# Kernel tuning notes

Hardware: AMD Instinct MI355X
Metric: run time of the kernel (lower is better)

Reference implementation:

```python
import jax, jax.numpy as jnp
import numpy as np

B, N, C = 4, 2048, 1024


def setup_inputs() -> dict:
    key = jax.random.key(0)
    ks = jax.random.split(key, 5)
    s = 1.0 / np.sqrt(C)
    return {
        "event_f": jax.random.normal(ks[0], (B, N, C), dtype=jnp.float32),
        "img_f": jax.random.normal(ks[1], (B, N, C), dtype=jnp.float32),
        "Wq": jax.random.normal(ks[2], (C, C), dtype=jnp.float32) * s,
        "bq": jnp.zeros((C,), dtype=jnp.float32),
        "Wk": jax.random.normal(ks[3], (C, C), dtype=jnp.float32) * s,
        "bk": jnp.zeros((C,), dtype=jnp.float32),
        "Wv": jax.random.normal(ks[4], (C, C), dtype=jnp.float32) * s,
        "bv": jnp.zeros((C,), dtype=jnp.float32),
    }


def reference(event_f, img_f, Wq, bq, Wk, bk, Wv, bv):
    # pointwise projections (conv_query/key/val as 1x1 / Linear C->C)
    q = jnp.einsum("bnc,cd->bnd", event_f, Wq) + bq  # [B,N,C]
    k = jnp.einsum("bnc,cd->bnd", img_f, Wk) + bk
    v = jnp.einsum("bnc,cd->bnd", img_f, Wv) + bv
    scale = 1.0 / jnp.sqrt(jnp.asarray(q.shape[-1], dtype=q.dtype))
    scores = jnp.einsum("bqc,bkc->bqk", q, k) * scale  # [B,N,N]
    p_attn = jax.nn.softmax(scores, axis=-1)
    return jnp.einsum("bqk,bkc->bqc", p_attn, v)  # [B,N,C]
```

## Files before the change

### kernel.cpp

```cpp
#include <hip/hip_runtime.h>
#include <hip/hip_bf16.h>
#include <stdint.h>

typedef __bf16 bf16;
typedef __attribute__((ext_vector_type(8))) __bf16 bf16x8;
typedef __attribute__((ext_vector_type(4))) float f32x4;

typedef __attribute__((address_space(3))) char* lds_ptr;
typedef const __attribute__((address_space(1))) char* glb_ptr;

#define BZ 4
#define NN 2048
#define CC 1024

__device__ __forceinline__ void gload_lds16(const bf16* g, bf16* l) {
    __builtin_amdgcn_global_load_lds((glb_ptr)g, (lds_ptr)l, 16, 0, 0);
}

__device__ __forceinline__ void bar() {
    asm volatile("" ::: "memory");
    __builtin_amdgcn_s_barrier();
    asm volatile("" ::: "memory");
}

__global__ void cvt2_f32_bf16(const float* __restrict__ a, const float* __restrict__ b,
                              bf16* __restrict__ oa, bf16* __restrict__ ob, int n8) {
    int i = blockIdx.x * blockDim.x + threadIdx.x;
    if (i >= 2 * n8) return;
    const float4* p;
    bf16* dst;
    int j;
    if (i < n8) { p = (const float4*)a; dst = oa; j = i; }
    else        { p = (const float4*)b; dst = ob; j = i - n8; }
    float4 x = p[2 * j], y = p[2 * j + 1];
    bf16x8 o;
    o[0] = (bf16)x.x; o[1] = (bf16)x.y; o[2] = (bf16)x.z; o[3] = (bf16)x.w;
    o[4] = (bf16)y.x; o[5] = (bf16)y.y; o[6] = (bf16)y.z; o[7] = (bf16)y.w;
    *(bf16x8*)(dst + 8 * (size_t)j) = o;
}

__global__ void transposeW3(const float* __restrict__ W0, const float* __restrict__ W1,
                            const float* __restrict__ W2, bf16* __restrict__ T0,
                            bf16* __restrict__ T1, bf16* __restrict__ T2) {
    __shared__ bf16 t[32][33];
    const int z = blockIdx.z;
    const float* W = z == 0 ? W0 : (z == 1 ? W1 : W2);
    bf16* Wt = z == 0 ? T0 : (z == 1 ? T1 : T2);
    int d0 = blockIdx.x * 32, c0 = blockIdx.y * 32;
    int tx = threadIdx.x, ty = threadIdx.y;
#pragma unroll
    for (int i = 0; i < 4; i++)
        t[ty + 8 * i][tx] = (bf16)W[(size_t)(c0 + ty + 8 * i) * CC + d0 + tx];
    __syncthreads();
#pragma unroll
    for (int i = 0; i < 4; i++)
        Wt[(size_t)(d0 + ty + 8 * i) * CC + c0 + tx] = t[tx][ty + 8 * i];
}

__global__ void prep(const float* __restrict__ a, const float* __restrict__ b,
                     float* __restrict__ bqk, float* __restrict__ rowsum) {
    int i = blockIdx.x * blockDim.x + threadIdx.x;
    rowsum[i] = 0.f;
    if (i < CC) bqk[i] = a[i];
    else if (i < 2 * CC) bqk[i] = b[i - CC];
}


#define STAGE_A(kt_, hh_)                                                        \
    do {                                                                         \
        int _kt = (kt_);                                                         \
        if (_kt < nkt) {                                                         \
            const bf16* _s = gAs + (size_t)((hh_)*128) * lda + (size_t)_kt * 64; \
            bf16* _d = &LA[_kt & 1][((hh_)*128 + wid * 16) * 64];                \
            gload_lds16(_s, _d);                                                 \
            gload_lds16(_s + (size_t)8 * lda, _d + 8 * 64);                      \
        }                                                                        \
    } while (0)

#define STAGE_B(kt_, hh_)                                                          \
    do {                                                                           \
        int _kt = (kt_);                                                           \
        if (_kt < nkt) {                                                           \
            const bf16* _s = gBs + (size_t)((hh_) * (BN / 2)) * ldb +              \
                             (size_t)_kt * 64;                                     \
            bf16* _d = &LB[_kt & 1][((hh_) * (BN / 2) + wid * (BN / 16)) * 64];    \
            gload_lds16(_s, _d);                                                   \
            if (NJ == 2) gload_lds16(_s + (size_t)8 * ldb, _d + 8 * 64);           \
        }                                                                          \
    } while (0)

#define LDA_FRAG(buf_, mh_)                                                      \
    do {                                                                         \
        _Pragma("unroll") for (int _i = 0; _i < 4; ++_i)                         \
            _Pragma("unroll") for (int _ks = 0; _ks < 2; ++_ks)                  \
                a[_i][_ks] = *(const bf16x8*)&LA[buf_][                          \
                    (wm + (mh_)*64 + _i * 16 + fr) * 64 +                        \
                    (((_ks * 4 + hi) ^ lo) * 8)];                                \
    } while (0)

#define LDB_FRAG(buf_, nh_, dst_)                                                \
    do {                                                                         \
        _Pragma("unroll") for (int _j = 0; _j < NJ; ++_j)                        \
            _Pragma("unroll") for (int _ks = 0; _ks < 2; ++_ks)                  \
                dst_[_j][_ks] = *(const bf16x8*)&LB[buf_][                       \
                    (wn + (nh_) * (NJ * 16) + _j * 16 + fr) * 64 +               \
                    (((_ks * 4 + hi) ^ lo) * 8)];                                \
    } while (0)

#define MMQ(mh_, nh_, b_)                                                        \
    do {                                                                         \
        __builtin_amdgcn_s_setprio(1);                                           \
        _Pragma("unroll") for (int _i = 0; _i < 4; ++_i)                         \
            _Pragma("unroll") for (int _j = 0; _j < NJ; ++_j)                    \
                _Pragma("unroll") for (int _ks = 0; _ks < 2; ++_ks)              \
                    acc[(mh_)*4 + _i][(nh_)*NJ + _j] =                           \
                        __builtin_amdgcn_mfma_f32_16x16x32_bf16(                 \
                            a[_i][_ks], b_[_j][_ks],                             \
                            acc[(mh_)*4 + _i][(nh_)*NJ + _j], 0, 0, 0);          \
        __builtin_amdgcn_s_setprio(0);                                           \
    } while (0)

#define VM_STEADY()                                                              \
    do {                                                                         \
        if (NJ == 2)                                                             \
            asm volatile("s_waitcnt vmcnt(6)" ::: "memory");                     \
        else                                                                     \
            asm volatile("s_waitcnt vmcnt(4)" ::: "memory");                     \
    } while (0)

template <int BN, int EPI, bool OUT_F32>
__global__ __launch_bounds__(512, 2) void gemm8(
    const bf16* __restrict__ A, int lda,
    const bf16* __restrict__ Bt, int ldb,
    void* __restrict__ Cout, int ldc,
    float* __restrict__ aux, long long sAux, float scale,
    long long sA, long long sB, long long sC, int nkt) {
    constexpr int NJ = BN / 128;
    __shared__ __align__(16) bf16 LA[2][256 * 64];
    __shared__ __align__(16) bf16 LB[2][BN * 64];

    const int nx = gridDim.x, ny = gridDim.y;
    const int nwg = nx * ny * gridDim.z;
    const int orig = blockIdx.x + nx * (blockIdx.y + ny * blockIdx.z);
    const int q = nwg >> 3, r = nwg & 7;
    const int xcd = orig & 7, land = orig >> 3;
    const int swz = (xcd < r ? xcd * (q + 1) : r * (q + 1) + (xcd - r) * q) + land;
    const int bx = swz % nx;
    const int tmp = swz / nx;
    const int by = tmp % ny, bz = tmp / ny;

    A += (size_t)bz * sA;
    Bt += (size_t)bz * sB;
    const int m0 = by * 256, n0 = bx * BN;
    const int t = threadIdx.x, wid = t >> 6, lane = t & 63;
    const int wm = (wid >> 2) * 128, wn = (wid & 3) * (BN / 4);
    const int fr = lane & 15, hi = lane >> 4, lo = lane & 7;
    f32x4 acc[8][2 * NJ] = {};

    const int srow = lane >> 3;
    const int schunk = lo ^ srow;
    const bf16* gAs = A + (size_t)(m0 + wid * 16 + srow) * lda + schunk * 8;
    const bf16* gBs = Bt + (size_t)(n0 + wid * (BN / 16) + srow) * ldb + schunk * 8;

    STAGE_A(0, 0); STAGE_A(0, 1); STAGE_B(0, 0); STAGE_B(0, 1);
    STAGE_B(1, 0); STAGE_A(1, 0); STAGE_B(1, 1);
    VM_STEADY();
    bar();

    bf16x8 a[4][2], b0[NJ][2], b1[NJ][2];
    for (int kt = 0; kt < nkt; ++kt) {
        const int buf = kt & 1;
        LDA_FRAG(buf, 0);
        LDB_FRAG(buf, 0, b0);
        STAGE_A(kt + 1, 1);
        MMQ(0, 0, b0);
        bar();
        LDB_FRAG(buf, 1, b1);
        MMQ(0, 1, b1);
        bar();
        LDA_FRAG(buf, 1);
        STAGE_B(kt + 2, 0);
        MMQ(1, 1, b1);
        bar();
        STAGE_A(kt + 2, 0);
        STAGE_B(kt + 2, 1);
        MMQ(1, 0, b0);
        if (kt + 2 < nkt)
            VM_STEADY();
        else
            asm volatile("s_waitcnt vmcnt(0)" ::: "memory");
        bar();
    }

    const int rq = hi * 4;
#pragma unroll
    for (int mh = 0; mh < 2; mh++)
#pragma unroll
        for (int i = 0; i < 4; i++) {
            const int row = m0 + wm + mh * 64 + i * 16 + rq;
            float rsum[4] = {0.f, 0.f, 0.f, 0.f};
            float inv[4];
            if (EPI == 4) {
#pragma unroll
                for (int rr = 0; rr < 4; rr++)
                    inv[rr] = 1.f / aux[bz * sAux + row + rr];
            }
#pragma unroll
            for (int nh = 0; nh < 2; nh++)
#pragma unroll
                for (int j = 0; j < NJ; j++) {
                    int col = n0 + wn + nh * (NJ * 16) + j * 16 + fr;
                    float bb = (EPI == 1) ? aux[bz * sAux + col] : 0.f;
                    f32x4 v = acc[mh * 4 + i][nh * NJ + j];
#pragma unroll
                    for (int rr = 0; rr < 4; rr++) {
                        float o = v[rr] * scale + bb;
                        if (EPI == 2) o += aux[row + rr];
                        if (EPI == 3) { o = __expf(o - 6.f); rsum[rr] += o; }
                        if (EPI == 4) o *= inv[rr];
                        if (OUT_F32)
                            ((float*)Cout)[(size_t)bz * sC + (size_t)(row + rr) * ldc + col] = o;
                        else
                            ((bf16*)Cout)[(size_t)bz * sC + (size_t)(row + rr) * ldc + col] = (bf16)o;
                    }
                }
            if (EPI == 3) {
#pragma unroll
                for (int rr = 0; rr < 4; rr++) {
                    float s = rsum[rr];
                    s += __shfl_xor(s, 1);
                    s += __shfl_xor(s, 2);
                    s += __shfl_xor(s, 4);
                    s += __shfl_xor(s, 8);
                    if (fr == 0) atomicAdd(&aux[bz * sAux + row + rr], s);
                }
            }
        }
}

extern "C" void kernel_launch(void* const* d_in, const int* in_sizes, int n_in,
                              void* d_out, int out_size, void* d_ws, size_t ws_size,
                              hipStream_t stream) {
    const float* event_f = (const float*)d_in[0];
    const float* img_f   = (const float*)d_in[1];
    const float* Wq = (const float*)d_in[2];
    const float* bq = (const float*)d_in[3];
    const float* Wk = (const float*)d_in[4];
    const float* bk = (const float*)d_in[5];
    const float* Wv = (const float*)d_in[6];
    const float* bv = (const float*)d_in[7];
    float* out = (float*)d_out;

    bf16* ws = (bf16*)d_ws;
    const size_t MC = (size_t)BZ * NN * CC;
    const size_t CCsq = (size_t)CC * CC;
    bf16* Ebf  = ws;
    bf16* Ibf  = ws + MC;
    bf16* S    = ws;
    size_t off = 2 * MC;
    bf16* Wqkt = ws + off; off += 2 * CCsq;
    bf16* Wvt  = ws + off; off += CCsq;
    bf16* Qb   = ws + off; off += MC;
    bf16* Kb   = ws + off; off += MC;
    bf16* VT   = ws + off; off += MC;
    float* bqk = (float*)(ws + off);
    float* rowsum = bqk + 2 * CC;

    {
        int n8 = (int)(MC / 8);
        cvt2_f32_bf16<<<dim3((2 * n8 + 255) / 256), dim3(256), 0, stream>>>(
            event_f, img_f, Ebf, Ibf, n8);
    }
    transposeW3<<<dim3(CC / 32, CC / 32, 3), dim3(32, 8), 0, stream>>>(
        Wq, Wk, Wv, Wqkt, Wqkt + CCsq, Wvt);
    prep<<<dim3(BZ * NN / 256), dim3(256), 0, stream>>>(bq, bk, bqk, rowsum);
    gemm8<128, 1, false><<<dim3(CC / 128, (BZ * NN) / 256, 2), dim3(512), 0, stream>>>(
        Ebf, CC, Wqkt, CC, Qb, CC, bqk, CC, 1.f,
        (long long)MC, (long long)CCsq, (long long)MC, CC / 64);
    gemm8<128, 2, false><<<dim3(NN / 128, CC / 256, BZ), dim3(512), 0, stream>>>(
        Wvt, CC, Ibf, CC, VT, NN, (float*)bv, 0, 1.f,
        0, (long long)NN * CC, (long long)CC * NN, CC / 64);
    gemm8<256, 3, false><<<dim3(NN / 256, NN / 256, BZ), dim3(512), 0, stream>>>(
        Qb, CC, Kb, CC, S, NN, rowsum, NN, 1.f / 32.f,
        (long long)NN * CC, (long long)NN * CC, (long long)NN * NN, CC / 64);
    gemm8<128, 4, true><<<dim3(CC / 128, NN / 256, BZ), dim3(512), 0, stream>>>(
        S, NN, VT, NN, out, CC, rowsum, NN, 1.f,
        (long long)NN * NN, (long long)CC * NN, (long long)NN * CC, NN / 64);
}
```

Before: 176.8 us.

## Shrink GEMM tiles to 128x128 with 256 threads and single-buffered B

Replaces the 256xBN tile, 512-thread GEMM with a 128x128 tile run by 256 threads (4 waves, each computing 64x64). The B tile loses its double buffer and is staged one k-step ahead inside the loop, with extra vmcnt waits and barriers. This cuts LDS use so three workgroups can share a CU and gives more blocks per launch. In exchange, operand reuse per loaded byte drops and the single B buffer adds stalls to the load/compute pipeline.

```diff
diff --git a/kernel.cpp b/kernel.cpp
--- a/kernel.cpp
+++ b/kernel.cpp
@@ -70,74 +70,66 @@
     do {                                                                         \
         int _kt = (kt_);                                                         \
         if (_kt < nkt) {                                                         \
-            const bf16* _s = gAs + (size_t)((hh_)*128) * lda + (size_t)_kt * 64; \
-            bf16* _d = &LA[_kt & 1][((hh_)*128 + wid * 16) * 64];                \
+            const bf16* _s = gAs + (size_t)((hh_)*64) * lda + (size_t)_kt * 64;  \
+            bf16* _d = &LA[_kt & 1][((hh_)*64 + wid * 16) * 64];                 \
             gload_lds16(_s, _d);                                                 \
             gload_lds16(_s + (size_t)8 * lda, _d + 8 * 64);                      \
         }                                                                        \
     } while (0)
 
-#define STAGE_B(kt_, hh_)                                                          \
-    do {                                                                           \
-        int _kt = (kt_);                                                           \
-        if (_kt < nkt) {                                                           \
-            const bf16* _s = gBs + (size_t)((hh_) * (BN / 2)) * ldb +              \
-                             (size_t)_kt * 64;                                     \
-            bf16* _d = &LB[_kt & 1][((hh_) * (BN / 2) + wid * (BN / 16)) * 64];    \
-            gload_lds16(_s, _d);                                                   \
-            if (NJ == 2) gload_lds16(_s + (size_t)8 * ldb, _d + 8 * 64);           \
-        }                                                                          \
+#define STAGE_B(kt_, hh_)                                                        \
+    do {                                                                         \
+        int _kt = (kt_);                                                         \
+        if (_kt < nkt) {                                                         \
+            const bf16* _s = gBs + (size_t)((hh_)*32) * ldb + (size_t)_kt * 64;  \
+            bf16* _d = &LB[((hh_)*32 + sbase) * 64];                             \
+            gload_lds16(_s, _d);                                                 \
+            gload_lds16(_s + (size_t)8 * ldb, _d + 8 * 64);                      \
+        }                                                                        \
     } while (0)
 
 #define LDA_FRAG(buf_, mh_)                                                      \
     do {                                                                         \
-        _Pragma("unroll") for (int _i = 0; _i < 4; ++_i)                         \
+        _Pragma("unroll") for (int _i = 0; _i < 2; ++_i)                         \
             _Pragma("unroll") for (int _ks = 0; _ks < 2; ++_ks)                  \
                 a[_i][_ks] = *(const bf16x8*)&LA[buf_][                          \
-                    (wm + (mh_)*64 + _i * 16 + fr) * 64 +                        \
+                    (wm + (mh_)*32 + _i * 16 + fr) * 64 +                        \
                     (((_ks * 4 + hi) ^ lo) * 8)];                                \
     } while (0)
 
-#define LDB_FRAG(buf_, nh_, dst_)                                                \
-    do {                                                                         \
-        _Pragma("unroll") for (int _j = 0; _j < NJ; ++_j)                        \
+#define LDB_FRAG(nh_, dst_)                                                      \
+    do {                                                                         \
+        _Pragma("unroll") for (int _j = 0; _j < 2; ++_j)                         \
             _Pragma("unroll") for (int _ks = 0; _ks < 2; ++_ks)                  \
-                dst_[_j][_ks] = *(const bf16x8*)&LB[buf_][                       \
-                    (wn + (nh_) * (NJ * 16) + _j * 16 + fr) * 64 +               \
+                dst_[_j][_ks] = *(const bf16x8*)&LB[                             \
+                    (wn + (nh_)*32 + _j * 16 + fr) * 64 +                        \
                     (((_ks * 4 + hi) ^ lo) * 8)];                                \
     } while (0)
 
 #define MMQ(mh_, nh_, b_)                                                        \
     do {                                                                         \
         __builtin_amdgcn_s_setprio(1);                                           \
-        _Pragma("unroll") for (int _i = 0; _i < 4; ++_i)                         \
-            _Pragma("unroll") for (int _j = 0; _j < NJ; ++_j)                    \
+        _Pragma("unroll") for (int _i = 0; _i < 2; ++_i)                         \
+            _Pragma("unroll") for (int _j = 0; _j < 2; ++_j)                     \
                 _Pragma("unroll") for (int _ks = 0; _ks < 2; ++_ks)              \
-                    acc[(mh_)*4 + _i][(nh_)*NJ + _j] =                           \
+                    acc[(mh_)*2 + _i][(nh_)*2 + _j] =                            \
                         __builtin_amdgcn_mfma_f32_16x16x32_bf16(                 \
                             a[_i][_ks], b_[_j][_ks],                             \
-                            acc[(mh_)*4 + _i][(nh_)*NJ + _j], 0, 0, 0);          \
+                            acc[(mh_)*2 + _i][(nh_)*2 + _j], 0, 0, 0);           \
         __builtin_amdgcn_s_setprio(0);                                           \
     } while (0)
 
-#define VM_STEADY()                                                              \
-    do {                                                                         \
-        if (NJ == 2)                                                             \
-            asm volatile("s_waitcnt vmcnt(6)" ::: "memory");                     \
-        else                                                                     \
-            asm volatile("s_waitcnt vmcnt(4)" ::: "memory");                     \
-    } while (0)
-
-template <int BN, int EPI, bool OUT_F32>
-__global__ __launch_bounds__(512, 2) void gemm8(
+#define VMW(n_) asm volatile("s_waitcnt vmcnt(" #n_ ")" ::: "memory")
+
+template <int EPI, bool OUT_F32>
+__global__ __launch_bounds__(256, 3) void gemm8(
     const bf16* __restrict__ A, int lda,
     const bf16* __restrict__ Bt, int ldb,
     void* __restrict__ Cout, int ldc,
     float* __restrict__ aux, long long sAux, float scale,
     long long sA, long long sB, long long sC, int nkt) {
-    constexpr int NJ = BN / 128;
-    __shared__ __align__(16) bf16 LA[2][256 * 64];
-    __shared__ __align__(16) bf16 LB[2][BN * 64];
+    __shared__ __align__(16) bf16 LA[2][128 * 64];
+    __shared__ __align__(16) bf16 LB[128 * 64];
 
     const int nx = gridDim.x, ny = gridDim.y;
     const int nwg = nx * ny * gridDim.z;
@@ -151,44 +143,46 @@
 
     A += (size_t)bz * sA;
     Bt += (size_t)bz * sB;
-    const int m0 = by * 256, n0 = bx * BN;
+    const int m0 = by * 128, n0 = bx * 128;
     const int t = threadIdx.x, wid = t >> 6, lane = t & 63;
-    const int wm = (wid >> 2) * 128, wn = (wid & 3) * (BN / 4);
+    const int wm = (wid >> 1) * 64, wn = (wid & 1) * 64;
     const int fr = lane & 15, hi = lane >> 4, lo = lane & 7;
-    f32x4 acc[8][2 * NJ] = {};
+    f32x4 acc[4][4] = {};
 
     const int srow = lane >> 3;
     const int schunk = lo ^ srow;
+    const int sbase = (wid >> 1) * 64 + (wid & 1) * 16;
     const bf16* gAs = A + (size_t)(m0 + wid * 16 + srow) * lda + schunk * 8;
-    const bf16* gBs = Bt + (size_t)(n0 + wid * (BN / 16) + srow) * ldb + schunk * 8;
+    const bf16* gBs = Bt + (size_t)(n0 + sbase + srow) * ldb + schunk * 8;
 
     STAGE_A(0, 0); STAGE_A(0, 1); STAGE_B(0, 0); STAGE_B(0, 1);
-    STAGE_B(1, 0); STAGE_A(1, 0); STAGE_B(1, 1);
-    VM_STEADY();
+    STAGE_A(1, 0);
+    if (nkt > 1) VMW(4); else VMW(2);
     bar();
 
-    bf16x8 a[4][2], b0[NJ][2], b1[NJ][2];
+    bf16x8 a[2][2], b0[2][2], b1[2][2];
     for (int kt = 0; kt < nkt; ++kt) {
         const int buf = kt & 1;
         LDA_FRAG(buf, 0);
-        LDB_FRAG(buf, 0, b0);
+        LDB_FRAG(0, b0);
         STAGE_A(kt + 1, 1);
         MMQ(0, 0, b0);
-        bar();
-        LDB_FRAG(buf, 1, b1);
+        if (kt + 1 < nkt) VMW(4);
+        else VMW(0);
+        bar();
+        LDB_FRAG(1, b1);
         MMQ(0, 1, b1);
         bar();
         LDA_FRAG(buf, 1);
-        STAGE_B(kt + 2, 0);
+        STAGE_B(kt + 1, 0);
         MMQ(1, 1, b1);
         bar();
+        STAGE_B(kt + 1, 1);
         STAGE_A(kt + 2, 0);
-        STAGE_B(kt + 2, 1);
         MMQ(1, 0, b0);
-        if (kt + 2 < nkt)
-            VM_STEADY();
-        else
-            asm volatile("s_waitcnt vmcnt(0)" ::: "memory");
+        if (kt + 2 < nkt) VMW(4);
+        else if (kt + 1 < nkt) VMW(2);
+        else VMW(0);
         bar();
     }
 
@@ -196,8 +190,8 @@
 #pragma unroll
     for (int mh = 0; mh < 2; mh++)
 #pragma unroll
-        for (int i = 0; i < 4; i++) {
-            const int row = m0 + wm + mh * 64 + i * 16 + rq;
+        for (int i = 0; i < 2; i++) {
+            const int row = m0 + wm + mh * 32 + i * 16 + rq;
             float rsum[4] = {0.f, 0.f, 0.f, 0.f};
             float inv[4];
             if (EPI == 4) {
@@ -208,10 +202,10 @@
 #pragma unroll
             for (int nh = 0; nh < 2; nh++)
 #pragma unroll
-                for (int j = 0; j < NJ; j++) {
-                    int col = n0 + wn + nh * (NJ * 16) + j * 16 + fr;
+                for (int j = 0; j < 2; j++) {
+                    int col = n0 + wn + nh * 32 + j * 16 + fr;
                     float bb = (EPI == 1) ? aux[bz * sAux + col] : 0.f;
-                    f32x4 v = acc[mh * 4 + i][nh * NJ + j];
+                    f32x4 v = acc[mh * 2 + i][nh * 2 + j];
 #pragma unroll
                     for (int rr = 0; rr < 4; rr++) {
                         float o = v[rr] * scale + bb;
@@ -274,16 +268,16 @@
     transposeW3<<<dim3(CC / 32, CC / 32, 3), dim3(32, 8), 0, stream>>>(
         Wq, Wk, Wv, Wqkt, Wqkt + CCsq, Wvt);
     prep<<<dim3(BZ * NN / 256), dim3(256), 0, stream>>>(bq, bk, bqk, rowsum);
-    gemm8<128, 1, false><<<dim3(CC / 128, (BZ * NN) / 256, 2), dim3(512), 0, stream>>>(
+    gemm8<1, false><<<dim3(CC / 128, (BZ * NN) / 128, 2), dim3(256), 0, stream>>>(
         Ebf, CC, Wqkt, CC, Qb, CC, bqk, CC, 1.f,
         (long long)MC, (long long)CCsq, (long long)MC, CC / 64);
-    gemm8<128, 2, false><<<dim3(NN / 128, CC / 256, BZ), dim3(512), 0, stream>>>(
+    gemm8<2, false><<<dim3(NN / 128, CC / 128, BZ), dim3(256), 0, stream>>>(
         Wvt, CC, Ibf, CC, VT, NN, (float*)bv, 0, 1.f,
         0, (long long)NN * CC, (long long)CC * NN, CC / 64);
-    gemm8<256, 3, false><<<dim3(NN / 256, NN / 256, BZ), dim3(512), 0, stream>>>(
+    gemm8<3, false><<<dim3(NN / 128, NN / 128, BZ), dim3(256), 0, stream>>>(
         Qb, CC, Kb, CC, S, NN, rowsum, NN, 1.f / 32.f,
         (long long)NN * CC, (long long)NN * CC, (long long)NN * NN, CC / 64);
-    gemm8<128, 4, true><<<dim3(CC / 128, NN / 256, BZ), dim3(512), 0, stream>>>(
+    gemm8<4, true><<<dim3(CC / 128, NN / 128, BZ), dim3(256), 0, stream>>>(
         S, NN, VT, NN, out, CC, rowsum, NN, 1.f,
         (long long)NN * NN, (long long)CC * NN, (long long)NN * CC, NN / 64);
 }
```

Measured after the change: 177.0 us. Within noise of the previous version (+0.1%).
